# Kernel tuning notes

Measured on AMD Instinct MI355X. Metric: run time of the kernel, lower is better.

The kernel has to match this reference:

```python
import jax, jax.numpy as jnp
import numpy as np

B, S, HID = 2, 2048, 2048
H, KH, D = 16, 4, 128  # heads, kv heads, head_dim
N_REP = H // KH
SCALE = D ** -0.5


def rotate_half(x):
    x1, x2 = x[..., : D // 2], x[..., D // 2:]
    return jnp.concatenate((-x2, x1), axis=-1)


def setup_inputs() -> dict:
    key = jax.random.key(0)
    ks = jax.random.split(key, 6)
    hidden_states = jax.random.normal(ks[0], (B, S, HID), jnp.float32)
    # standard RoPE cos/sin tables, shape [B, S, D]
    inv_freq = 1.0 / (10000.0 ** (np.arange(0, D, 2, dtype=np.float32) / D))
    pos = np.arange(S, dtype=np.float32)
    freqs = np.outer(pos, inv_freq)            # [S, D/2]
    emb = np.concatenate([freqs, freqs], -1)   # [S, D]
    cos = jnp.broadcast_to(jnp.cos(emb), (B, S, D)).astype(jnp.float32)
    sin = jnp.broadcast_to(jnp.sin(emb), (B, S, D)).astype(jnp.float32)
    # additive causal mask [1, 1, S, S]
    neg = jnp.finfo(jnp.float32).min
    causal = jnp.triu(jnp.full((S, S), neg, jnp.float32), k=1)
    attention_mask = causal[None, None]
    std = 0.02
    wq = jax.random.normal(ks[1], (HID, H * D), jnp.float32) * std
    wk = jax.random.normal(ks[2], (HID, KH * D), jnp.float32) * std
    wv = jax.random.normal(ks[3], (HID, KH * D), jnp.float32) * std
    wo = jax.random.normal(ks[4], (H * D, HID), jnp.float32) * std
    return {"hidden_states": hidden_states, "cos": cos, "sin": sin,
            "attention_mask": attention_mask, "wq": wq, "wk": wk, "wv": wv, "wo": wo}


def reference(hidden_states, cos, sin, attention_mask, wq, wk, wv, wo):
    b, s, _ = hidden_states.shape
    q = (hidden_states @ wq).reshape(b, s, H, D).transpose(0, 2, 1, 3)   # [b,H,s,d]
    k = (hidden_states @ wk).reshape(b, s, KH, D).transpose(0, 2, 1, 3)  # [b,KH,s,d]
    v = (hidden_states @ wv).reshape(b, s, KH, D).transpose(0, 2, 1, 3)
    c = cos[:, None, :, :]  # [b,1,s,d] broadcast over heads
    sn = sin[:, None, :, :]
    q = q * c + rotate_half(q) * sn
    k = k * c + rotate_half(k) * sn
    # GQA: repeat KV heads
    k = jnp.repeat(k, N_REP, axis=1)  # [b,H,s,d]
    v = jnp.repeat(v, N_REP, axis=1)
    scores = jnp.einsum('bhqd,bhkd->bhqk', q, k) * SCALE + attention_mask
    probs = jax.nn.softmax(scores, axis=-1)
    attn = jnp.einsum('bhqk,bhkd->bhqd', probs, v)
    attn = attn.transpose(0, 2, 1, 3).reshape(b, s, H * D)
    return attn @ wo
```

## Files before the change

### kernel.cpp

```cpp
#include <hip/hip_runtime.h>
#include <stdint.h>

#define Bc   2
#define Sc   2048
#define HIDc 2048
#define Hc   16
#define KHc  4
#define Dc   128
#define HDc  2048
#define KHDc 512
#define QKVS 3072
#define SCALE2c 0.12751744657f
#define N_ITEMS 1536

typedef _Float16 f16;
typedef _Float16 f16x2 __attribute__((ext_vector_type(2)));
typedef _Float16 f16x4 __attribute__((ext_vector_type(4)));
typedef _Float16 f16x8 __attribute__((ext_vector_type(8)));
typedef float    f32x4 __attribute__((ext_vector_type(4)));

__device__ __forceinline__ void gl_lds16(const void* g, void* l) {
  __builtin_amdgcn_global_load_lds(
      (const __attribute__((address_space(1))) unsigned int*)g,
      (__attribute__((address_space(3))) unsigned int*)l, 16, 0, 0);
}

__global__ __launch_bounds__(256) void conv_hs(const float* __restrict__ in,
                                               f16* __restrict__ out,
                                               int* __restrict__ ctr) {
  if (blockIdx.x == 0 && threadIdx.x == 0) *ctr = 0;
  int i = (blockIdx.x * 256 + threadIdx.x) * 4;
  float4 v = *(const float4*)&in[i];
  f16x4 o; o[0] = (f16)v.x; o[1] = (f16)v.y; o[2] = (f16)v.z; o[3] = (f16)v.w;
  *(f16x4*)&out[i] = o;
}

__global__ __launch_bounds__(256) void trw_all(const float* __restrict__ wq,
                                               const float* __restrict__ wk,
                                               const float* __restrict__ wv,
                                               const float* __restrict__ wo,
                                               f16* __restrict__ wqkvT,
                                               f16* __restrict__ woT) {
  const int z = blockIdx.z;
  const float* in; f16* out; int C, rowOff;
  if (z == 0)      { in = wq; out = wqkvT; C = 2048; rowOff = 0; }
  else if (z == 1) { in = wk; out = wqkvT; C = 512;  rowOff = 2048; }
  else if (z == 2) { in = wv; out = wqkvT; C = 512;  rowOff = 2560; }
  else             { in = wo; out = woT;   C = 2048; rowOff = 0; }
  if (blockIdx.x * 64 >= C) return;
  __shared__ float Ld[64 * 65];
  const int tid = threadIdx.x;
  const int r0 = blockIdx.y * 64, c0 = blockIdx.x * 64;
#pragma unroll
  for (int p = 0; p < 4; ++p) {
    int idx = p * 256 + tid;
    int r = idx >> 4, c4 = (idx & 15) * 4;
    float4 v = *(const float4*)&in[(size_t)(r0 + r) * C + c0 + c4];
    Ld[r * 65 + c4 + 0] = v.x; Ld[r * 65 + c4 + 1] = v.y;
    Ld[r * 65 + c4 + 2] = v.z; Ld[r * 65 + c4 + 3] = v.w;
  }
  __syncthreads();
#pragma unroll
  for (int p = 0; p < 4; ++p) {
    int idx = p * 256 + tid;
    int oc = idx >> 4, m4 = (idx & 15) * 4;
    f16x4 o;
#pragma unroll
    for (int i = 0; i < 4; ++i) o[i] = (f16)Ld[(m4 + i) * 65 + oc];
    *(f16x4*)&out[(size_t)(rowOff + c0 + oc) * 2048 + r0 + m4] = o;
  }
}

__global__ __launch_bounds__(256) void rope_all(f16* __restrict__ x,
                                                const float* __restrict__ cb,
                                                const float* __restrict__ sb) {
  int bid = blockIdx.x;
  int colbase, log2h, idx;
  if (bid < 16384) { colbase = 0;    log2h = 4; idx = bid * 256 + threadIdx.x; }
  else             { colbase = 2048; log2h = 2; idx = (bid - 16384) * 256 + threadIdx.x; }
  int d   = idx & 63;
  int h   = (idx >> 6) & ((1 << log2h) - 1);
  int row = idx >> (6 + log2h);
  f16* p = x + (size_t)row * QKVS + colbase + h * 128;
  float x1 = (float)p[d], x2 = (float)p[64 + d];
  float c = cb[(size_t)row * 128 + d], s = sb[(size_t)row * 128 + d];
  p[d]      = (f16)(x1 * c - x2 * s);
  p[64 + d] = (f16)(x2 * c + x1 * s);
}

__global__ __launch_bounds__(256) void v_tr(const f16* __restrict__ QKV,
                                            f16* __restrict__ Vt) {
  __shared__ f16 Ld[64 * 78];
  const int tid = threadIdx.x;
  const int s0 = blockIdx.x * 64, d0 = blockIdx.y * 64;
  const int b = blockIdx.z >> 2, kh = blockIdx.z & 3;
#pragma unroll
  for (int p = 0; p < 2; ++p) {
    int idx = p * 256 + tid;
    int sl = idx >> 3, dc8 = (idx & 7) * 8;
    f16x8 v = *(const f16x8*)&QKV[(size_t)(b * Sc + s0 + sl) * QKVS + 2560 + kh * 128 + d0 + dc8];
#pragma unroll
    for (int i = 0; i < 4; ++i) {
      f16x2 w; w[0] = v[2 * i]; w[1] = v[2 * i + 1];
      *(f16x2*)&Ld[sl * 78 + dc8 + 2 * i] = w;
    }
  }
  __syncthreads();
  {
    int dr = (tid >> 3) * 2, sc8 = (tid & 7) * 8;
    f16x8 r0v, r1v;
#pragma unroll
    for (int j = 0; j < 8; ++j) {
      f16x2 w = *(const f16x2*)&Ld[(sc8 + j) * 78 + dr];
      r0v[j] = w[0]; r1v[j] = w[1];
    }
    size_t obase = ((size_t)(b * KHc + kh) * 128 + d0 + dr) * Sc + s0 + sc8;
    *(f16x8*)&Vt[obase]      = r0v;
    *(f16x8*)&Vt[obase + Sc] = r1v;
  }
}

__global__ __launch_bounds__(256) void gemm_bt(const f16* __restrict__ A,
                                               const f16* __restrict__ Bt,
                                               void* __restrict__ Cout,
                                               int M, int N, int K, int c_f16) {
  __shared__ f16 Al[128 * 64];
  __shared__ f16 Bl[128 * 64];
  const int tid  = threadIdx.x;
  const int lane = tid & 63, wave = tid >> 6;
  const int quad = lane >> 4, l16 = lane & 15;
  const int wm = (wave >> 1) * 64, wn = (wave & 1) * 64;
  const int m0 = blockIdx.y * 128, n0 = blockIdx.x * 128;
  f32x4 acc[4][4] = {};

  for (int k0 = 0; k0 < K; k0 += 64) {
    __syncthreads();
#pragma unroll
    for (int p = 0; p < 4; ++p) {
      const int g  = wave * 2 + (p >> 1);
      const int kq = (p & 1) * 4 + quad;
      gl_lds16(&A [(size_t)(m0 + g * 16 + l16) * K + k0 + kq * 8], &Al[(wave * 4 + p) * 512]);
      gl_lds16(&Bt[(size_t)(n0 + g * 16 + l16) * K + k0 + kq * 8], &Bl[(wave * 4 + p) * 512]);
    }
    __syncthreads();
#pragma unroll
    for (int ks = 0; ks < 2; ++ks) {
      f16x8 af[4], bf[4];
#pragma unroll
      for (int i = 0; i < 4; ++i)
        af[i] = *(const f16x8*)&Al[((((wave >> 1) * 4 + i) * 8 + ks * 4 + quad) * 16 + l16) * 8];
#pragma unroll
      for (int j = 0; j < 4; ++j)
        bf[j] = *(const f16x8*)&Bl[((((wave & 1) * 4 + j) * 8 + ks * 4 + quad) * 16 + l16) * 8];
#pragma unroll
      for (int i = 0; i < 4; ++i)
#pragma unroll
        for (int j = 0; j < 4; ++j)
          acc[i][j] = __builtin_amdgcn_mfma_f32_16x16x32_f16(af[i], bf[j], acc[i][j], 0, 0, 0);
    }
  }

  if (c_f16) {
    f16* C = (f16*)Cout;
#pragma unroll
    for (int i = 0; i < 4; ++i)
#pragma unroll
      for (int j = 0; j < 4; ++j)
#pragma unroll
        for (int r = 0; r < 4; ++r)
          C[(size_t)(m0 + wm + i * 16 + quad * 4 + r) * N + n0 + wn + j * 16 + l16] =
              (f16)acc[i][j][r];
  } else {
    float* C = (float*)Cout;
#pragma unroll
    for (int i = 0; i < 4; ++i)
#pragma unroll
      for (int j = 0; j < 4; ++j)
#pragma unroll
        for (int r = 0; r < 4; ++r)
          C[(size_t)(m0 + wm + i * 16 + quad * 4 + r) * N + n0 + wn + j * 16 + l16] =
              acc[i][j][r];
  }
}

__global__ __launch_bounds__(256) void gemm_qkv96(const f16* __restrict__ A,
                                                  const f16* __restrict__ Bt,
                                                  f16* __restrict__ C) {
  __shared__ f16 Al[128 * 64];
  __shared__ f16 Bl[96 * 64];
  const int tid  = threadIdx.x;
  const int lane = tid & 63, wave = tid >> 6;
  const int quad = lane >> 4, l16 = lane & 15;
  const int wm = (wave >> 1) * 64;
  const int wnG = (wave & 1) * 3;
  const int m0 = blockIdx.y * 128, n0 = blockIdx.x * 96;
  const int K = 2048;
  f32x4 acc[4][3] = {};

  for (int k0 = 0; k0 < K; k0 += 64) {
    __syncthreads();
#pragma unroll
    for (int p = 0; p < 4; ++p) {
      const int g  = wave * 2 + (p >> 1);
      const int kq = (p & 1) * 4 + quad;
      gl_lds16(&A[(size_t)(m0 + g * 16 + l16) * K + k0 + kq * 8], &Al[(wave * 4 + p) * 512]);
    }
#pragma unroll
    for (int p = 0; p < 3; ++p) {
      const int gb = wave * 3 + p;
      const int gi = gb >> 1, kh2 = gb & 1;
      gl_lds16(&Bt[(size_t)(n0 + gi * 16 + l16) * K + k0 + kh2 * 32 + quad * 8], &Bl[gb * 512]);
    }
    __syncthreads();
#pragma unroll
    for (int ks = 0; ks < 2; ++ks) {
      f16x8 af[4], bf[3];
#pragma unroll
      for (int i = 0; i < 4; ++i)
        af[i] = *(const f16x8*)&Al[((((wave >> 1) * 4 + i) * 8 + ks * 4 + quad) * 16 + l16) * 8];
#pragma unroll
      for (int j = 0; j < 3; ++j)
        bf[j] = *(const f16x8*)&Bl[(((wnG + j) * 8 + ks * 4 + quad) * 16 + l16) * 8];
#pragma unroll
      for (int i = 0; i < 4; ++i)
#pragma unroll
        for (int j = 0; j < 3; ++j)
          acc[i][j] = __builtin_amdgcn_mfma_f32_16x16x32_f16(af[i], bf[j], acc[i][j], 0, 0, 0);
    }
  }

#pragma unroll
  for (int i = 0; i < 4; ++i)
#pragma unroll
    for (int j = 0; j < 3; ++j)
#pragma unroll
      for (int r = 0; r < 4; ++r)
        C[(size_t)(m0 + wm + i * 16 + quad * 4 + r) * QKVS + n0 + (wnG + j) * 16 + l16] =
            (f16)acc[i][j][r];
}

__global__ __launch_bounds__(256, 4) void attn_v4(const f16* __restrict__ QKV,
                                                  const f16* __restrict__ Vt,
                                                  f16* __restrict__ Ob,
                                                  f16* __restrict__ Opart,
                                                  float2* __restrict__ ML,
                                                  int* __restrict__ ctr) {
  __shared__ f16 Kl[64 * 128];
  __shared__ f16 Vl[64 * 128];
  __shared__ f16 Ps[4 * 512];
  __shared__ int item_s;
  const int tid  = threadIdx.x;
  const int lane = tid & 63, wave = tid >> 6;
  const int quad = lane >> 4, l16 = lane & 15;

  f16x8 ones_f;
#pragma unroll
  for (int i = 0; i < 8; ++i) ones_f[i] = (l16 == 0) ? (f16)1.0f : (f16)0.0f;

  for (;;) {
    if (tid == 0) item_s = atomicAdd(ctr, 1);
    __syncthreads();
    const int item = item_s;
    if (item >= N_ITEMS) break;

    int qt, bh, k0t, k1t, hf = -1;
    if (item < 1280) {
      int base = 0, c = 32;
#pragma unroll 1
      for (; c >= 17; --c) {
        int sz = (c & 1) ? 64 : 96;
        if (item < base + sz) break;
        base += sz;
      }
      int off = item - base;
      if (off < 64) {
        qt = c - 1; hf = off >> 5; bh = off & 31;
        int nk = qt + 1, hn = nk >> 1;
        k0t = hf ? hn : 0; k1t = hf ? nk : hn;
      } else {
        qt = (c >> 1) - 1; bh = off - 64; k0t = 0; k1t = qt + 1;
      }
    } else {
      int off = item - 1280;
      qt = 7 - (off >> 5); bh = off & 31; k0t = 0; k1t = qt + 1;
    }
    const int b = bh >> 4, h = bh & 15, kh = h >> 2;
    const int qbase = qt * 64 + wave * 16;

    f16x8 qf[4];
    {
      const f16* qp = QKV + (size_t)(b * Sc + qbase + l16) * QKVS + h * 128 + quad * 8;
#pragma unroll
      for (int c = 0; c < 4; ++c) qf[c] = *(const f16x8*)(qp + c * 32);
    }
    float m_i[4] = {-1e30f, -1e30f, -1e30f, -1e30f};
    f32x4 ls = {};
    f32x4 o[8] = {};

    for (int kt = k0t; kt < k1t; ++kt) {
      __syncthreads();
#pragma unroll
      for (int p = 0; p < 4; ++p) {
        gl_lds16(&QKV[(size_t)(b * Sc + kt * 64 + wave * 16 + l16) * QKVS + 2048 + kh * 128 + p * 32 + quad * 8],
                 &Kl[(wave * 4 + p) * 512]);
        const int dt = wave * 2 + (p >> 1), kc = p & 1;
        gl_lds16(&Vt[(size_t)((b * KHc + kh) * 128 + dt * 16 + l16) * Sc + kt * 64 + kc * 32 + quad * 8],
                 &Vl[(wave * 4 + p) * 512]);
      }
      __syncthreads();

      f32x4 s[4] = {};
#pragma unroll
      for (int kc = 0; kc < 2; ++kc)
#pragma unroll
        for (int c = 0; c < 4; ++c) {
          f16x8 ka = *(const f16x8*)&Kl[(((kc * 2 + 0) * 4 + c) * 4 + quad) * 128 + l16 * 8];
          f16x8 kb = *(const f16x8*)&Kl[(((kc * 2 + 1) * 4 + c) * 4 + quad) * 128 + l16 * 8];
          s[kc * 2 + 0] = __builtin_amdgcn_mfma_f32_16x16x32_f16(qf[c], ka, s[kc * 2 + 0], 0, 0, 0);
          s[kc * 2 + 1] = __builtin_amdgcn_mfma_f32_16x16x32_f16(qf[c], kb, s[kc * 2 + 1], 0, 0, 0);
        }

      const int cb = kt * 64 + l16;
      const int wb = wave * 512 + (l16 & 7);
      const int rhi = l16 >> 3;
      float e2[4], e3[4], alpha[4];
#pragma unroll
      for (int r = 0; r < 4; ++r) {
        int qrow = qbase + quad * 4 + r;
        float v0 = s[0][r] * SCALE2c, v1 = s[1][r] * SCALE2c;
        float v2 = s[2][r] * SCALE2c, v3 = s[3][r] * SCALE2c;
        if (cb      > qrow) v0 = -1e30f;
        if (cb + 16 > qrow) v1 = -1e30f;
        if (cb + 32 > qrow) v2 = -1e30f;
        if (cb + 48 > qrow) v3 = -1e30f;
        float mx = fmaxf(fmaxf(v0, v1), fmaxf(v2, v3));
        mx = fmaxf(mx, __shfl_xor(mx, 1));
        mx = fmaxf(mx, __shfl_xor(mx, 2));
        mx = fmaxf(mx, __shfl_xor(mx, 4));
        mx = fmaxf(mx, __shfl_xor(mx, 8));
        float mnew = fmaxf(m_i[r], mx);
        alpha[r] = exp2f(m_i[r] - mnew);
        m_i[r] = mnew;
        v0 = exp2f(v0 - mnew); v1 = exp2f(v1 - mnew);
        v2 = exp2f(v2 - mnew); v3 = exp2f(v3 - mnew);
        int rowoff = (quad * 4 + r) * 8;
        Ps[wb + (rhi + 0) * 128 + rowoff] = (f16)v0;
        Ps[wb + (rhi + 2) * 128 + rowoff] = (f16)v1;
        e2[r] = v2; e3[r] = v3;
      }
#pragma unroll
      for (int r = 0; r < 4; ++r) ls[r] *= alpha[r];
#pragma unroll
      for (int dt = 0; dt < 8; ++dt)
#pragma unroll
        for (int r = 0; r < 4; ++r) o[dt][r] *= alpha[r];

      {
        f16x8 pf = *(const f16x8*)&Ps[wave * 512 + quad * 128 + l16 * 8];
        ls = __builtin_amdgcn_mfma_f32_16x16x32_f16(pf, ones_f, ls, 0, 0, 0);
#pragma unroll
        for (int dt = 0; dt < 8; ++dt) {
          f16x8 vf = *(const f16x8*)&Vl[((dt * 2 + 0) * 4 + quad) * 128 + l16 * 8];
          o[dt] = __builtin_amdgcn_mfma_f32_16x16x32_f16(pf, vf, o[dt], 0, 0, 0);
        }
      }
#pragma unroll
      for (int r = 0; r < 4; ++r) {
        int rowoff = (quad * 4 + r) * 8;
        Ps[wb + (rhi + 0) * 128 + rowoff] = (f16)e2[r];
        Ps[wb + (rhi + 2) * 128 + rowoff] = (f16)e3[r];
      }
      {
        f16x8 pf = *(const f16x8*)&Ps[wave * 512 + quad * 128 + l16 * 8];
        ls = __builtin_amdgcn_mfma_f32_16x16x32_f16(pf, ones_f, ls, 0, 0, 0);
#pragma unroll
        for (int dt = 0; dt < 8; ++dt) {
          f16x8 vf = *(const f16x8*)&Vl[((dt * 2 + 1) * 4 + quad) * 128 + l16 * 8];
          o[dt] = __builtin_amdgcn_mfma_f32_16x16x32_f16(pf, vf, o[dt], 0, 0, 0);
        }
      }
    }

    float inv[4], lrow[4];
#pragma unroll
    for (int r = 0; r < 4; ++r) {
      lrow[r] = __shfl(ls[r], lane & 48);
      inv[r] = 1.0f / lrow[r];
    }
    if (hf < 0) {
#pragma unroll
      for (int dt = 0; dt < 8; ++dt)
#pragma unroll
        for (int r = 0; r < 4; ++r)
          Ob[(size_t)(b * Sc + qbase + quad * 4 + r) * HDc + h * 128 + dt * 16 + l16] =
              (f16)(o[dt][r] * inv[r]);
    } else {
      const int tile = (qt - 16) * 32 + bh;
      f16* op = Opart + ((size_t)tile * 2 + hf) * (64 * 128);
#pragma unroll
      for (int dt = 0; dt < 8; ++dt)
#pragma unroll
        for (int r = 0; r < 4; ++r)
          op[(wave * 16 + quad * 4 + r) * 128 + dt * 16 + l16] = (f16)(o[dt][r] * inv[r]);
      if (l16 == 0) {
#pragma unroll
        for (int r = 0; r < 4; ++r) {
          float2 ml; ml.x = m_i[r]; ml.y = lrow[r];
          ML[((size_t)tile * 2 + hf) * 64 + wave * 16 + quad * 4 + r] = ml;
        }
      }
    }
  }
}

__global__ __launch_bounds__(256) void attn_merge(const f16* __restrict__ Opart,
                                                  const float2* __restrict__ ML,
                                                  f16* __restrict__ Ob) {
  const int tile = blockIdx.x;
  const int qt = 16 + (tile >> 5), bh = tile & 31;
  const int b = bh >> 4, h = bh & 15;
  const int tid = threadIdx.x;
  const int row = tid >> 2, c0 = (tid & 3) * 32;
  float2 ml1 = ML[(size_t)tile * 2 * 64 + row];
  float2 ml2 = ML[((size_t)tile * 2 + 1) * 64 + row];
  float m = fmaxf(ml1.x, ml2.x);
  float w1 = ml1.y * exp2f(ml1.x - m);
  float w2 = ml2.y * exp2f(ml2.x - m);
  float rinv = 1.0f / (w1 + w2);
  float a1 = w1 * rinv, a2 = w2 * rinv;
  const f16* o1 = Opart + (size_t)tile * 2 * (64 * 128) + row * 128 + c0;
  const f16* o2 = o1 + 64 * 128;
  f16* out = Ob + (size_t)(b * Sc + qt * 64 + row) * HDc + h * 128 + c0;
#pragma unroll
  for (int j = 0; j < 4; ++j) {
    f16x8 x1 = *(const f16x8*)(o1 + j * 8);
    f16x8 x2 = *(const f16x8*)(o2 + j * 8);
    f16x8 y;
#pragma unroll
    for (int i = 0; i < 8; ++i) y[i] = (f16)(a1 * (float)x1[i] + a2 * (float)x2[i]);
    *(f16x8*)(out + j * 8) = y;
  }
}

extern "C" void kernel_launch(void* const* d_in, const int* in_sizes, int n_in,
                              void* d_out, int out_size, void* d_ws, size_t ws_size,
                              hipStream_t stream) {
  (void)in_sizes; (void)n_in; (void)out_size; (void)ws_size;
  const float* hs   = (const float*)d_in[0];
  const float* cosb = (const float*)d_in[1];
  const float* sinb = (const float*)d_in[2];
  const float* wq = (const float*)d_in[4];
  const float* wk = (const float*)d_in[5];
  const float* wv = (const float*)d_in[6];
  const float* wo = (const float*)d_in[7];
  float* out = (float*)d_out;

  char* ws = (char*)d_ws;
  int*  ctr = (int*)ws;
  size_t off = 256;
  auto alloc = [&](size_t bytes) { char* p = ws + off; off += (bytes + 255) & ~(size_t)255; return p; };
  f16*  hsF   = (f16*)alloc((size_t)Bc * Sc * HIDc * 2);
  f16*  woT   = (f16*)alloc((size_t)HIDc * HDc * 2);
  f16*  QKVf  = (f16*)alloc((size_t)Bc * Sc * QKVS * 2);
  f16*  Vt_g  = (f16*)alloc((size_t)Bc * KHc * Dc * Sc * 2);
  f16*  wqkvT = (f16*)alloc((size_t)QKVS * HIDc * 2);
  f16*  Opart = wqkvT;
  {
    size_t opart_bytes = (size_t)512 * 2 * 64 * 128 * 2;
    size_t wqkvT_bytes = (size_t)QKVS * HIDc * 2;
    if (opart_bytes > wqkvT_bytes) off += opart_bytes - wqkvT_bytes;
  }
  float2* ML = (float2*)alloc((size_t)512 * 2 * 64 * sizeof(float2));
  f16*  attnF = hsF;

  conv_hs<<<8192, 256, 0, stream>>>(hs, hsF, ctr);
  trw_all<<<dim3(32, 32, 4), 256, 0, stream>>>(wq, wk, wv, wo, wqkvT, woT);

  gemm_qkv96<<<dim3(32, 32), 256, 0, stream>>>(hsF, wqkvT, QKVf);

  rope_all<<<20480, 256, 0, stream>>>(QKVf, cosb, sinb);
  v_tr<<<dim3(32, 2, 8), 256, 0, stream>>>(QKVf, Vt_g);

  attn_v4<<<1024, 256, 0, stream>>>(QKVf, Vt_g, attnF, Opart, ML, ctr);
  attn_merge<<<512, 256, 0, stream>>>(Opart, ML, attnF);

  gemm_bt<<<dim3(16, 32), 256, 0, stream>>>(attnF, woT, out, 4096, 2048, 2048, 0);
}
```

Baseline: 442.4 us.

## Restructure attention to two waves of 32 rows with staged K/V prefetch

The attention kernel moves from four waves with 16 query rows each to two waves with 32 rows each, so every K/V fragment read from LDS feeds two MFMAs. The next tile's K load is issued after QK^T and its V load after PV, with vmcnt waits in place of the full sync-load-sync sequence, so global loads overlap compute. The causal mask now runs only on the diagonal tile, and the running-max rescale is skipped when the wave-wide max rises by no more than 8 (exp2 domain). Registers per thread roughly double and occupancy drops (launch bounds 128,2). Skipping the rescale lets unnormalized exponentials reach 256, which fp16 P values still hold.

```diff
diff --git a/kernel.cpp b/kernel.cpp
--- a/kernel.cpp
+++ b/kernel.cpp
@@ -239,7 +239,7 @@
             (f16)acc[i][j][r];
 }
 
-__global__ __launch_bounds__(256, 4) void attn_v4(const f16* __restrict__ QKV,
+__global__ __launch_bounds__(128, 2) void attn_v5(const f16* __restrict__ QKV,
                                                   const f16* __restrict__ Vt,
                                                   f16* __restrict__ Ob,
                                                   f16* __restrict__ Opart,
@@ -247,7 +247,7 @@
                                                   int* __restrict__ ctr) {
   __shared__ f16 Kl[64 * 128];
   __shared__ f16 Vl[64 * 128];
-  __shared__ f16 Ps[4 * 512];
+  __shared__ f16 Ps[2 * 2 * 512];
   __shared__ int item_s;
   const int tid  = threadIdx.x;
   const int lane = tid & 63, wave = tid >> 6;
@@ -285,128 +285,197 @@
       qt = 7 - (off >> 5); bh = off & 31; k0t = 0; k1t = qt + 1;
     }
     const int b = bh >> 4, h = bh & 15, kh = h >> 2;
-    const int qbase = qt * 64 + wave * 16;
-
-    f16x8 qf[4];
-    {
-      const f16* qp = QKV + (size_t)(b * Sc + qbase + l16) * QKVS + h * 128 + quad * 8;
-#pragma unroll
-      for (int c = 0; c < 4; ++c) qf[c] = *(const f16x8*)(qp + c * 32);
-    }
-    float m_i[4] = {-1e30f, -1e30f, -1e30f, -1e30f};
-    f32x4 ls = {};
-    f32x4 o[8] = {};
+    const int qbase = qt * 64 + wave * 32;
+
+    f16x8 qf[2][4];
+#pragma unroll
+    for (int rg = 0; rg < 2; ++rg) {
+      const f16* qp = QKV + (size_t)(b * Sc + qbase + rg * 16 + l16) * QKVS + h * 128 + quad * 8;
+#pragma unroll
+      for (int c = 0; c < 4; ++c) qf[rg][c] = *(const f16x8*)(qp + c * 32);
+    }
+    float m_i[2][4];
+#pragma unroll
+    for (int rg = 0; rg < 2; ++rg)
+#pragma unroll
+      for (int r = 0; r < 4; ++r) m_i[rg][r] = -1e30f;
+    f32x4 ls[2] = {};
+    f32x4 o[2][8] = {};
+
+    auto stageK = [&](int kt) {
+#pragma unroll
+      for (int p = 0; p < 8; ++p) {
+        const int g = wave * 8 + p, kg = g >> 2, dc = g & 3;
+        gl_lds16(&QKV[(size_t)(b * Sc + kt * 64 + kg * 16 + l16) * QKVS + 2048 + kh * 128 + dc * 32 + quad * 8],
+                 &Kl[g * 512]);
+      }
+    };
+    auto stageV = [&](int kt) {
+#pragma unroll
+      for (int p = 0; p < 8; ++p) {
+        const int g = wave * 8 + p, dt = g >> 1, kc = g & 1;
+        gl_lds16(&Vt[(size_t)((b * KHc + kh) * 128 + dt * 16 + l16) * Sc + kt * 64 + kc * 32 + quad * 8],
+                 &Vl[g * 512]);
+      }
+    };
+
+    stageK(k0t);
+    stageV(k0t);
 
     for (int kt = k0t; kt < k1t; ++kt) {
-      __syncthreads();
-#pragma unroll
-      for (int p = 0; p < 4; ++p) {
-        gl_lds16(&QKV[(size_t)(b * Sc + kt * 64 + wave * 16 + l16) * QKVS + 2048 + kh * 128 + p * 32 + quad * 8],
-                 &Kl[(wave * 4 + p) * 512]);
-        const int dt = wave * 2 + (p >> 1), kc = p & 1;
-        gl_lds16(&Vt[(size_t)((b * KHc + kh) * 128 + dt * 16 + l16) * Sc + kt * 64 + kc * 32 + quad * 8],
-                 &Vl[(wave * 4 + p) * 512]);
-      }
-      __syncthreads();
-
-      f32x4 s[4] = {};
+      const bool more = (kt + 1 < k1t);
+
+      asm volatile("s_waitcnt vmcnt(8)" ::: "memory");
+      __builtin_amdgcn_sched_barrier(0);
+      __builtin_amdgcn_s_barrier();
+      __builtin_amdgcn_sched_barrier(0);
+
+      f32x4 s[2][4] = {};
 #pragma unroll
       for (int kc = 0; kc < 2; ++kc)
 #pragma unroll
         for (int c = 0; c < 4; ++c) {
           f16x8 ka = *(const f16x8*)&Kl[(((kc * 2 + 0) * 4 + c) * 4 + quad) * 128 + l16 * 8];
           f16x8 kb = *(const f16x8*)&Kl[(((kc * 2 + 1) * 4 + c) * 4 + quad) * 128 + l16 * 8];
-          s[kc * 2 + 0] = __builtin_amdgcn_mfma_f32_16x16x32_f16(qf[c], ka, s[kc * 2 + 0], 0, 0, 0);
-          s[kc * 2 + 1] = __builtin_amdgcn_mfma_f32_16x16x32_f16(qf[c], kb, s[kc * 2 + 1], 0, 0, 0);
-        }
-
+          s[0][kc * 2 + 0] = __builtin_amdgcn_mfma_f32_16x16x32_f16(qf[0][c], ka, s[0][kc * 2 + 0], 0, 0, 0);
+          s[1][kc * 2 + 0] = __builtin_amdgcn_mfma_f32_16x16x32_f16(qf[1][c], ka, s[1][kc * 2 + 0], 0, 0, 0);
+          s[0][kc * 2 + 1] = __builtin_amdgcn_mfma_f32_16x16x32_f16(qf[0][c], kb, s[0][kc * 2 + 1], 0, 0, 0);
+          s[1][kc * 2 + 1] = __builtin_amdgcn_mfma_f32_16x16x32_f16(qf[1][c], kb, s[1][kc * 2 + 1], 0, 0, 0);
+        }
+      __builtin_amdgcn_sched_barrier(0);
+      __builtin_amdgcn_s_barrier();
+      __builtin_amdgcn_sched_barrier(0);
+      if (more) stageK(kt + 1);
+
+      const bool diag = (kt == qt);
       const int cb = kt * 64 + l16;
-      const int wb = wave * 512 + (l16 & 7);
-      const int rhi = l16 >> 3;
-      float e2[4], e3[4], alpha[4];
-#pragma unroll
-      for (int r = 0; r < 4; ++r) {
-        int qrow = qbase + quad * 4 + r;
-        float v0 = s[0][r] * SCALE2c, v1 = s[1][r] * SCALE2c;
-        float v2 = s[2][r] * SCALE2c, v3 = s[3][r] * SCALE2c;
-        if (cb      > qrow) v0 = -1e30f;
-        if (cb + 16 > qrow) v1 = -1e30f;
-        if (cb + 32 > qrow) v2 = -1e30f;
-        if (cb + 48 > qrow) v3 = -1e30f;
-        float mx = fmaxf(fmaxf(v0, v1), fmaxf(v2, v3));
-        mx = fmaxf(mx, __shfl_xor(mx, 1));
-        mx = fmaxf(mx, __shfl_xor(mx, 2));
-        mx = fmaxf(mx, __shfl_xor(mx, 4));
-        mx = fmaxf(mx, __shfl_xor(mx, 8));
-        float mnew = fmaxf(m_i[r], mx);
-        alpha[r] = exp2f(m_i[r] - mnew);
-        m_i[r] = mnew;
-        v0 = exp2f(v0 - mnew); v1 = exp2f(v1 - mnew);
-        v2 = exp2f(v2 - mnew); v3 = exp2f(v3 - mnew);
-        int rowoff = (quad * 4 + r) * 8;
-        Ps[wb + (rhi + 0) * 128 + rowoff] = (f16)v0;
-        Ps[wb + (rhi + 2) * 128 + rowoff] = (f16)v1;
-        e2[r] = v2; e3[r] = v3;
-      }
-#pragma unroll
-      for (int r = 0; r < 4; ++r) ls[r] *= alpha[r];
-#pragma unroll
-      for (int dt = 0; dt < 8; ++dt)
-#pragma unroll
-        for (int r = 0; r < 4; ++r) o[dt][r] *= alpha[r];
+      float e2[2][4], e3[2][4];
+#pragma unroll
+      for (int rg = 0; rg < 2; ++rg) {
+        float mx[4];
+#pragma unroll
+        for (int r = 0; r < 4; ++r) {
+          float v0 = s[rg][0][r] * SCALE2c, v1 = s[rg][1][r] * SCALE2c;
+          float v2 = s[rg][2][r] * SCALE2c, v3 = s[rg][3][r] * SCALE2c;
+          if (diag) {
+            const int qrow = qbase + rg * 16 + quad * 4 + r;
+            if (cb      > qrow) v0 = -1e30f;
+            if (cb + 16 > qrow) v1 = -1e30f;
+            if (cb + 32 > qrow) v2 = -1e30f;
+            if (cb + 48 > qrow) v3 = -1e30f;
+          }
+          s[rg][0][r] = v0; s[rg][1][r] = v1; s[rg][2][r] = v2; s[rg][3][r] = v3;
+          float m = fmaxf(fmaxf(v0, v1), fmaxf(v2, v3));
+          m = fmaxf(m, __shfl_xor(m, 1));
+          m = fmaxf(m, __shfl_xor(m, 2));
+          m = fmaxf(m, __shfl_xor(m, 4));
+          m = fmaxf(m, __shfl_xor(m, 8));
+          mx[r] = m;
+        }
+        float need = fmaxf(fmaxf(mx[0] - m_i[rg][0], mx[1] - m_i[rg][1]),
+                           fmaxf(mx[2] - m_i[rg][2], mx[3] - m_i[rg][3]));
+        if (!__all(need <= 8.0f)) {
+#pragma unroll
+          for (int r = 0; r < 4; ++r) {
+            float mnew = fmaxf(m_i[rg][r], mx[r]);
+            float a = exp2f(m_i[rg][r] - mnew);
+            m_i[rg][r] = mnew;
+            ls[rg][r] *= a;
+#pragma unroll
+            for (int dt = 0; dt < 8; ++dt) o[rg][dt][r] *= a;
+          }
+        }
+        const int wb  = wave * 1024 + rg * 512 + (l16 & 7);
+        const int rhi = l16 >> 3;
+#pragma unroll
+        for (int r = 0; r < 4; ++r) {
+          float p0 = exp2f(s[rg][0][r] - m_i[rg][r]);
+          float p1 = exp2f(s[rg][1][r] - m_i[rg][r]);
+          e2[rg][r] = exp2f(s[rg][2][r] - m_i[rg][r]);
+          e3[rg][r] = exp2f(s[rg][3][r] - m_i[rg][r]);
+          const int rowoff = (quad * 4 + r) * 8;
+          Ps[wb + (rhi + 0) * 128 + rowoff] = (f16)p0;
+          Ps[wb + (rhi + 2) * 128 + rowoff] = (f16)p1;
+        }
+      }
+
+      if (more) { asm volatile("s_waitcnt vmcnt(8)" ::: "memory"); }
+      else      { asm volatile("s_waitcnt vmcnt(0)" ::: "memory"); }
+      __builtin_amdgcn_sched_barrier(0);
+      __builtin_amdgcn_s_barrier();
+      __builtin_amdgcn_sched_barrier(0);
 
       {
-        f16x8 pf = *(const f16x8*)&Ps[wave * 512 + quad * 128 + l16 * 8];
-        ls = __builtin_amdgcn_mfma_f32_16x16x32_f16(pf, ones_f, ls, 0, 0, 0);
+        f16x8 pf0 = *(const f16x8*)&Ps[wave * 1024 +       quad * 128 + l16 * 8];
+        f16x8 pf1 = *(const f16x8*)&Ps[wave * 1024 + 512 + quad * 128 + l16 * 8];
+        ls[0] = __builtin_amdgcn_mfma_f32_16x16x32_f16(pf0, ones_f, ls[0], 0, 0, 0);
+        ls[1] = __builtin_amdgcn_mfma_f32_16x16x32_f16(pf1, ones_f, ls[1], 0, 0, 0);
 #pragma unroll
         for (int dt = 0; dt < 8; ++dt) {
           f16x8 vf = *(const f16x8*)&Vl[((dt * 2 + 0) * 4 + quad) * 128 + l16 * 8];
-          o[dt] = __builtin_amdgcn_mfma_f32_16x16x32_f16(pf, vf, o[dt], 0, 0, 0);
-        }
-      }
-#pragma unroll
-      for (int r = 0; r < 4; ++r) {
-        int rowoff = (quad * 4 + r) * 8;
-        Ps[wb + (rhi + 0) * 128 + rowoff] = (f16)e2[r];
-        Ps[wb + (rhi + 2) * 128 + rowoff] = (f16)e3[r];
+          o[0][dt] = __builtin_amdgcn_mfma_f32_16x16x32_f16(pf0, vf, o[0][dt], 0, 0, 0);
+          o[1][dt] = __builtin_amdgcn_mfma_f32_16x16x32_f16(pf1, vf, o[1][dt], 0, 0, 0);
+        }
+      }
+#pragma unroll
+      for (int rg = 0; rg < 2; ++rg) {
+        const int wb  = wave * 1024 + rg * 512 + (l16 & 7);
+        const int rhi = l16 >> 3;
+#pragma unroll
+        for (int r = 0; r < 4; ++r) {
+          const int rowoff = (quad * 4 + r) * 8;
+          Ps[wb + (rhi + 0) * 128 + rowoff] = (f16)e2[rg][r];
+          Ps[wb + (rhi + 2) * 128 + rowoff] = (f16)e3[rg][r];
+        }
       }
       {
-        f16x8 pf = *(const f16x8*)&Ps[wave * 512 + quad * 128 + l16 * 8];
-        ls = __builtin_amdgcn_mfma_f32_16x16x32_f16(pf, ones_f, ls, 0, 0, 0);
+        f16x8 pf0 = *(const f16x8*)&Ps[wave * 1024 +       quad * 128 + l16 * 8];
+        f16x8 pf1 = *(const f16x8*)&Ps[wave * 1024 + 512 + quad * 128 + l16 * 8];
+        ls[0] = __builtin_amdgcn_mfma_f32_16x16x32_f16(pf0, ones_f, ls[0], 0, 0, 0);
+        ls[1] = __builtin_amdgcn_mfma_f32_16x16x32_f16(pf1, ones_f, ls[1], 0, 0, 0);
 #pragma unroll
         for (int dt = 0; dt < 8; ++dt) {
           f16x8 vf = *(const f16x8*)&Vl[((dt * 2 + 1) * 4 + quad) * 128 + l16 * 8];
-          o[dt] = __builtin_amdgcn_mfma_f32_16x16x32_f16(pf, vf, o[dt], 0, 0, 0);
-        }
-      }
-    }
-
-    float inv[4], lrow[4];
-#pragma unroll
-    for (int r = 0; r < 4; ++r) {
-      lrow[r] = __shfl(ls[r], lane & 48);
-      inv[r] = 1.0f / lrow[r];
-    }
-    if (hf < 0) {
-#pragma unroll
-      for (int dt = 0; dt < 8; ++dt)
-#pragma unroll
-        for (int r = 0; r < 4; ++r)
-          Ob[(size_t)(b * Sc + qbase + quad * 4 + r) * HDc + h * 128 + dt * 16 + l16] =
-              (f16)(o[dt][r] * inv[r]);
-    } else {
-      const int tile = (qt - 16) * 32 + bh;
-      f16* op = Opart + ((size_t)tile * 2 + hf) * (64 * 128);
-#pragma unroll
-      for (int dt = 0; dt < 8; ++dt)
-#pragma unroll
-        for (int r = 0; r < 4; ++r)
-          op[(wave * 16 + quad * 4 + r) * 128 + dt * 16 + l16] = (f16)(o[dt][r] * inv[r]);
-      if (l16 == 0) {
-#pragma unroll
-        for (int r = 0; r < 4; ++r) {
-          float2 ml; ml.x = m_i[r]; ml.y = lrow[r];
-          ML[((size_t)tile * 2 + hf) * 64 + wave * 16 + quad * 4 + r] = ml;
+          o[0][dt] = __builtin_amdgcn_mfma_f32_16x16x32_f16(pf0, vf, o[0][dt], 0, 0, 0);
+          o[1][dt] = __builtin_amdgcn_mfma_f32_16x16x32_f16(pf1, vf, o[1][dt], 0, 0, 0);
+        }
+      }
+      __builtin_amdgcn_sched_barrier(0);
+      __builtin_amdgcn_s_barrier();
+      __builtin_amdgcn_sched_barrier(0);
+      if (more) stageV(kt + 1);
+    }
+
+#pragma unroll
+    for (int rg = 0; rg < 2; ++rg) {
+      float inv[4], lrow[4];
+#pragma unroll
+      for (int r = 0; r < 4; ++r) {
+        lrow[r] = __shfl(ls[rg][r], lane & 48);
+        inv[r] = 1.0f / lrow[r];
+      }
+      const int rl = wave * 32 + rg * 16 + quad * 4;
+      if (hf < 0) {
+#pragma unroll
+        for (int dt = 0; dt < 8; ++dt)
+#pragma unroll
+          for (int r = 0; r < 4; ++r)
+            Ob[(size_t)(b * Sc + qt * 64 + rl + r) * HDc + h * 128 + dt * 16 + l16] =
+                (f16)(o[rg][dt][r] * inv[r]);
+      } else {
+        const int tile = (qt - 16) * 32 + bh;
+        f16* op = Opart + ((size_t)tile * 2 + hf) * (64 * 128);
+#pragma unroll
+        for (int dt = 0; dt < 8; ++dt)
+#pragma unroll
+          for (int r = 0; r < 4; ++r)
+            op[(rl + r) * 128 + dt * 16 + l16] = (f16)(o[rg][dt][r] * inv[r]);
+        if (l16 == 0) {
+#pragma unroll
+          for (int r = 0; r < 4; ++r) {
+            float2 ml; ml.x = m_i[rg][r]; ml.y = lrow[r];
+            ML[((size_t)tile * 2 + hf) * 64 + rl + r] = ml;
+          }
         }
       }
     }
@@ -481,7 +550,7 @@
   rope_all<<<20480, 256, 0, stream>>>(QKVf, cosb, sinb);
   v_tr<<<dim3(32, 2, 8), 256, 0, stream>>>(QKVf, Vt_g);
 
-  attn_v4<<<1024, 256, 0, stream>>>(QKVf, Vt_g, attnF, Opart, ML, ctr);
+  attn_v5<<<1024, 128, 0, stream>>>(QKVf, Vt_g, attnF, Opart, ML, ctr);
   attn_merge<<<512, 256, 0, stream>>>(Opart, ML, attnF);
 
   gemm_bt<<<dim3(16, 32), 256, 0, stream>>>(attnF, woT, out, 4096, 2048, 2048, 0);
```

New measurement: 461.7 us. 1.04x slower.
